# Kernel tuning notes

Measured on AMD Instinct MI355X. Metric: run time of the kernel, lower is better.

## Reference

```python
import jax, jax.numpy as jnp
import numpy as np

B = 2
D_MODEL = 256
D_FFN = 1024
N_LEVELS = 4
N_HEADS = 8
N_POINTS = 4
D_HEAD = D_MODEL // N_HEADS
SHAPES = np.array([[128, 128], [64, 64], [32, 32], [16, 16]], dtype=np.int32)  # (H, W) per level
LEN = int(SHAPES.prod(axis=1).sum())  # 21760
EPS = 1e-5


def _layer_norm(x, g, b):
    m = jnp.mean(x, axis=-1, keepdims=True)
    v = jnp.mean(jnp.square(x - m), axis=-1, keepdims=True)
    return (x - m) * jax.lax.rsqrt(v + EPS) * g + b


def _bilinear_gather(v_l, loc, H, W):
    # v_l: [B, H*W, NH, DH]; loc: [B, L, NH, NP, 2] in normalized [0,1] coords (x, y)
    # grid_sample(align_corners=False, padding_mode=zeros) semantics: pixel = loc * size - 0.5
    x = loc[..., 0] * W - 0.5
    y = loc[..., 1] * H - 0.5
    x0 = jnp.floor(x)
    y0 = jnp.floor(y)
    dx = x - x0
    dy = y - y0
    x0i = x0.astype(jnp.int32)
    y0i = y0.astype(jnp.int32)
    b_ix = jnp.arange(v_l.shape[0])[:, None, None, None]
    h_ix = jnp.arange(v_l.shape[2])[None, None, :, None]

    def corner(xi, yi, w):
        valid = (xi >= 0) & (xi < W) & (yi >= 0) & (yi < H)
        idx = jnp.clip(yi, 0, H - 1) * W + jnp.clip(xi, 0, W - 1)
        v = v_l[b_ix, idx, h_ix]  # [B, L, NH, NP, DH]
        return v * (w * valid.astype(v.dtype))[..., None]

    return (corner(x0i, y0i, (1 - dx) * (1 - dy))
            + corner(x0i + 1, y0i, dx * (1 - dy))
            + corner(x0i, y0i + 1, (1 - dx) * dy)
            + corner(x0i + 1, y0i + 1, dx * dy))


def _forward(src, pos, reference_points,
             w_off, b_off, w_attn, b_attn, w_val, b_val, w_out, b_out,
             ln1_g, ln1_b, w1, b1, w2, b2, ln2_g, ln2_b,
             spatial_shapes, level_start_index, padding_mask):
    shapes = np.asarray(spatial_shapes)        # static per-level (H, W)
    starts = np.asarray(level_start_index)     # static level offsets
    Bsz, L, _ = src.shape

    # ---- MSDeformAttn ----
    q = src + pos                              # with_pos_embed
    value = src @ w_val + b_val
    value = jnp.where(padding_mask[..., None], 0.0, value)
    value = value.reshape(Bsz, L, N_HEADS, D_HEAD)

    off = (q @ w_off + b_off).reshape(Bsz, L, N_HEADS, N_LEVELS, N_POINTS, 2)
    attn = (q @ w_attn + b_attn).reshape(Bsz, L, N_HEADS, N_LEVELS * N_POINTS)
    attn = jax.nn.softmax(attn, axis=-1).reshape(Bsz, L, N_HEADS, N_LEVELS, N_POINTS)

    wh = jnp.asarray(shapes[:, ::-1].copy(), dtype=src.dtype)  # [NL, 2] = (W, H)
    loc = reference_points[:, :, None, :, None, :] + off / wh[None, None, None, :, None, :]

    out = jnp.zeros((Bsz, L, N_HEADS, D_HEAD), src.dtype)
    for l in range(N_LEVELS):
        H, W = int(shapes[l, 0]), int(shapes[l, 1])
        s = int(starts[l])
        v_l = value[:, s:s + H * W]                          # [B, H*W, NH, DH]
        sampled = _bilinear_gather(v_l, loc[:, :, :, l], H, W)  # [B, L, NH, NP, DH]
        out = out + (sampled * attn[:, :, :, l][..., None]).sum(axis=3)
    attn_out = out.reshape(Bsz, L, D_MODEL) @ w_out + b_out

    # ---- residual + LN + FFN + residual + LN (dropout = identity in eval) ----
    x = _layer_norm(src + attn_out, ln1_g, ln1_b)
    ffn = jax.nn.relu(x @ w1 + b1) @ w2 + b2
    return _layer_norm(x + ffn, ln2_g, ln2_b)


def setup_inputs() -> dict:
    key = jax.random.key(0)
    ks = jax.random.split(key, 16)
    s = 0.02
    n_off = N_HEADS * N_LEVELS * N_POINTS
    level_start = np.concatenate([[0], SHAPES.prod(axis=1).cumsum()[:-1]]).astype(np.int32)
    return {
        "src": jax.random.normal(ks[0], (B, LEN, D_MODEL), jnp.float32),
        "pos": jax.random.normal(ks[1], (B, LEN, D_MODEL), jnp.float32),
        "reference_points": jax.random.uniform(ks[2], (B, LEN, N_LEVELS, 2), jnp.float32),
        "spatial_shapes": jnp.asarray(SHAPES),
        "level_start_index": jnp.asarray(level_start),
        "padding_mask": jnp.zeros((B, LEN), jnp.bool_),
        "w_off": jax.random.normal(ks[3], (D_MODEL, n_off * 2), jnp.float32) * s,
        "b_off": jax.random.normal(ks[4], (n_off * 2,), jnp.float32) * 0.5,
        "w_attn": jax.random.normal(ks[5], (D_MODEL, n_off), jnp.float32) * s,
        "b_attn": jnp.zeros((n_off,), jnp.float32),
        "w_val": jax.random.normal(ks[6], (D_MODEL, D_MODEL), jnp.float32) * s,
        "b_val": jnp.zeros((D_MODEL,), jnp.float32),
        "w_out": jax.random.normal(ks[7], (D_MODEL, D_MODEL), jnp.float32) * s,
        "b_out": jnp.zeros((D_MODEL,), jnp.float32),
        "ln1_g": jnp.ones((D_MODEL,), jnp.float32),
        "ln1_b": jnp.zeros((D_MODEL,), jnp.float32),
        "w1": jax.random.normal(ks[8], (D_MODEL, D_FFN), jnp.float32) * s,
        "b1": jnp.zeros((D_FFN,), jnp.float32),
        "w2": jax.random.normal(ks[9], (D_FFN, D_MODEL), jnp.float32) * s,
        "b2": jnp.zeros((D_MODEL,), jnp.float32),
        "ln2_g": jnp.ones((D_MODEL,), jnp.float32),
        "ln2_b": jnp.zeros((D_MODEL,), jnp.float32),
    }


def reference(src, pos, reference_points, spatial_shapes, level_start_index, padding_mask,
              w_off, b_off, w_attn, b_attn, w_val, b_val, w_out, b_out,
              ln1_g, ln1_b, w1, b1, w2, b2, ln2_g, ln2_b):
    return _forward(src, pos, reference_points,
                    w_off, b_off, w_attn, b_attn, w_val, b_val, w_out, b_out,
                    ln1_g, ln1_b, w1, b1, w2, b2, ln2_g, ln2_b,
                    spatial_shapes, level_start_index, padding_mask)
```

## Files before the change

kernel.cpp:

```cpp
#include <hip/hip_runtime.h>
#include <hip/hip_bf16.h>

#define BSZ      2
#define LTOK     21760
#define NTOK     (BSZ * LTOK)
#define DMODEL   256
#define DFFN     1024

typedef __attribute__((ext_vector_type(8))) short short8;
typedef __attribute__((ext_vector_type(4))) float f32x4;

__device__ __forceinline__ unsigned short f2bf(float x) {
    __hip_bfloat16 h = __float2bfloat16(x);
    return *reinterpret_cast<unsigned short*>(&h);
}
__device__ __forceinline__ float bf2f(unsigned short u) {
    union { unsigned int i; float f; } c; c.i = ((unsigned int)u) << 16; return c.f;
}
__device__ __forceinline__ float bflo(unsigned int u) {
    union { unsigned int i; float f; } c; c.i = u << 16; return c.f;
}
__device__ __forceinline__ float bfhi(unsigned int u) {
    union { unsigned int i; float f; } c; c.i = u & 0xffff0000u; return c.f;
}

__device__ __forceinline__ void gload_lds16(const void* g, void* l) {
    __builtin_amdgcn_global_load_lds(
        (const __attribute__((address_space(1))) unsigned int*)g,
        (__attribute__((address_space(3))) unsigned int*)l, 16, 0, 0);
}

#define TM 128
#define TN 256
#define TBK 32
#define EBS 264

__device__ __forceinline__ void gemm_core(
    const unsigned short* __restrict__ A,
    const unsigned short* __restrict__ Bt,
    unsigned short* smem,
    int bm, int bn, int N, int K,
    int tid, int lane, int wm, int wn,
    f32x4 acc[4][4])
{
    const int sr = tid >> 6;
    const int fr = lane & 15;
    const int fk = (lane >> 4) * 8;

    const unsigned short* aR  = A  + (size_t)(bm + sr * 16 + fr) * K + fk;
    const unsigned short* bR0 = Bt + (size_t)min(bn + sr * 16 + fr,       N - 1) * K + fk;
    const unsigned short* bR1 = Bt + (size_t)min(bn + (sr + 8) * 16 + fr, N - 1) * K + fk;

    unsigned short* sA = smem;
    unsigned short* sB = smem + TM * TBK;

    for (int k0 = 0; k0 < K; k0 += TBK) {
        gload_lds16(aR  + k0, &sA[sr * 512]);
        gload_lds16(bR0 + k0, &sB[sr * 512]);
        gload_lds16(bR1 + k0, &sB[(sr + 8) * 512]);
        __syncthreads();

        short8 af[4], bfr[4];
        #pragma unroll
        for (int i = 0; i < 4; ++i)
            af[i] = *(const short8*)&sA[(wm * 4 + i) * 512 + lane * 8];
        #pragma unroll
        for (int j = 0; j < 4; ++j)
            bfr[j] = *(const short8*)&sB[(wn * 4 + j) * 512 + lane * 8];
        #pragma unroll
        for (int i = 0; i < 4; ++i)
            #pragma unroll
            for (int j = 0; j < 4; ++j)
                acc[i][j] = __builtin_amdgcn_mfma_f32_16x16x32_bf16(
                    af[i], bfr[j], acc[i][j], 0, 0, 0);
        __syncthreads();
    }
}

__global__ __launch_bounds__(512, 4) void gemm_mfma(
    const unsigned short* __restrict__ A,
    const unsigned short* __restrict__ Bt, const float* __restrict__ bias,
    unsigned short* __restrict__ Cb,
    int M, int N, int K, int relu)
{
    __shared__ __align__(16) unsigned short smem[TM * TBK + TN * TBK];
    const int tid  = threadIdx.x;
    const int lane = tid & 63;
    const int wave = tid >> 6;
    const int wm = wave >> 2, wn = wave & 3;
    const int bm = blockIdx.y * TM;
    const int bn = blockIdx.x * TN;

    f32x4 acc[4][4];
    #pragma unroll
    for (int i = 0; i < 4; ++i)
        #pragma unroll
        for (int j = 0; j < 4; ++j)
            acc[i][j] = (f32x4){0.f, 0.f, 0.f, 0.f};

    gemm_core(A, Bt, smem, bm, bn, N, K, tid, lane, wm, wn, acc);

    const int r0 = (lane >> 4) * 4;
    const int c0 = lane & 15;
    unsigned short* eb = smem;
    #pragma unroll
    for (int i = 0; i < 4; ++i) {
        if (i) __syncthreads();
        #pragma unroll
        for (int j = 0; j < 4; ++j) {
            const int col = bn + wn * 64 + j * 16 + c0;
            const float bj = (col < N) ? bias[col] : 0.f;
            #pragma unroll
            for (int r = 0; r < 4; ++r) {
                float v = acc[i][j][r] + bj;
                if (relu) v = fmaxf(v, 0.f);
                eb[(wm * 16 + r0 + r) * EBS + wn * 64 + j * 16 + c0] = f2bf(v);
            }
        }
        __syncthreads();
        #pragma unroll
        for (int qq = 0; qq < 2; ++qq) {
            const int q  = tid + qq * 512;
            const int rl = q >> 5;
            const int ch = q & 31;
            const int grow = bm + (rl >> 4) * 64 + i * 16 + (rl & 15);
            const int colb = bn + ch * 8;
            if (colb < N)
                *(uint4*)&Cb[(size_t)grow * N + colb] =
                    *(const uint4*)&eb[rl * EBS + ch * 8];
        }
    }
}

__global__ __launch_bounds__(512, 4) void gemm_proj(
    const unsigned short* __restrict__ A0, const unsigned short* __restrict__ B0,
    const float* __restrict__ bias0, unsigned short* __restrict__ C0,
    const unsigned char* __restrict__ mask,
    const unsigned short* __restrict__ A1, const unsigned short* __restrict__ B1,
    const float* __restrict__ bias1, unsigned short* __restrict__ C1)
{
    __shared__ __align__(16) unsigned short smem[TM * TBK + TN * TBK];
    const int tid  = threadIdx.x;
    const int lane = tid & 63;
    const int wave = tid >> 6;
    const int wm = wave >> 2, wn = wave & 3;
    const int bm = blockIdx.y * TM;
    const int bx = blockIdx.x;

    const int isv = (bx == 0);
    const unsigned short* A    = isv ? A0 : A1;
    const unsigned short* Bt   = isv ? B0 : B1;
    const float*          bias = isv ? bias0 : bias1;
    const int N  = isv ? 256 : 384;
    const int bn = isv ? 0 : (bx - 1) * 256;
    const int K  = 256;

    f32x4 acc[4][4];
    #pragma unroll
    for (int i = 0; i < 4; ++i)
        #pragma unroll
        for (int j = 0; j < 4; ++j)
            acc[i][j] = (f32x4){0.f, 0.f, 0.f, 0.f};

    gemm_core(A, Bt, smem, bm, bn, N, K, tid, lane, wm, wn, acc);

    const int r0 = (lane >> 4) * 4;
    const int c0 = lane & 15;
    unsigned short* eb = smem;
    #pragma unroll
    for (int i = 0; i < 4; ++i) {
        if (i) __syncthreads();
        #pragma unroll
        for (int j = 0; j < 4; ++j) {
            const int col = bn + wn * 64 + j * 16 + c0;
            const float bj = (col < N) ? bias[col] : 0.f;
            #pragma unroll
            for (int r = 0; r < 4; ++r) {
                const int row = bm + wm * 64 + i * 16 + r0 + r;
                float v = acc[i][j][r] + bj;
                if (isv && mask[row]) v = 0.f;
                eb[(wm * 16 + r0 + r) * EBS + wn * 64 + j * 16 + c0] = f2bf(v);
            }
        }
        __syncthreads();
        #pragma unroll
        for (int qq = 0; qq < 2; ++qq) {
            const int q  = tid + qq * 512;
            const int rl = q >> 5;
            const int ch = q & 31;
            const int grow = bm + (rl >> 4) * 64 + i * 16 + (rl & 15);
            const int colb = bn + ch * 8;
            if (colb < N) {
                const uint4 val = *(const uint4*)&eb[rl * EBS + ch * 8];
                if (isv) {
                    const int bb   = grow >= LTOK;
                    const int srow = grow - bb * LTOK;
                    const int hcol = ch >> 2;
                    const int d    = (ch & 3) * 8;
                    *(uint4*)&C0[((size_t)(bb * 8 + hcol) * LTOK + srow) * 32 + d] = val;
                } else {
                    *(uint4*)&C1[(size_t)grow * 384 + colb] = val;
                }
            }
        }
    }
}

__global__ __launch_bounds__(512, 4) void gemm_ln(
    const unsigned short* __restrict__ A,
    const unsigned short* __restrict__ Bt, const float* __restrict__ bias,
    const unsigned short* __restrict__ resid,
    const float* __restrict__ g, const float* __restrict__ be,
    float* __restrict__ outF, unsigned short* __restrict__ outB, int K)
{
    __shared__ __align__(16) unsigned short smem[TM * TBK + TN * TBK];
    const int tid  = threadIdx.x;
    const int lane = tid & 63;
    const int wave = tid >> 6;
    const int wm = wave >> 2, wn = wave & 3;
    const int bm = blockIdx.y * TM;

    f32x4 acc[4][4];
    #pragma unroll
    for (int i = 0; i < 4; ++i)
        #pragma unroll
        for (int j = 0; j < 4; ++j)
            acc[i][j] = (f32x4){0.f, 0.f, 0.f, 0.f};

    gemm_core(A, Bt, smem, bm, 0, 256, K, tid, lane, wm, wn, acc);

    const int r0 = (lane >> 4) * 4;
    const int c0 = lane & 15;
    unsigned short* eb = smem;

    #pragma unroll
    for (int i = 0; i < 4; ++i) {
        if (i) __syncthreads();
        #pragma unroll
        for (int j = 0; j < 4; ++j) {
            const int col = wn * 64 + j * 16 + c0;
            const float bj = bias[col];
            #pragma unroll
            for (int r = 0; r < 4; ++r)
                eb[(wm * 16 + r0 + r) * EBS + col] = f2bf(acc[i][j][r] + bj);
        }
        __syncthreads();

        const int row = tid >> 4;
        const int l   = tid & 15;
        const int grow = bm + (row >> 4) * 64 + i * 16 + (row & 15);
        const unsigned short* rr = resid + (size_t)grow * 256 + l * 16;

        float s = 0.f, sq = 0.f;
        #pragma unroll
        for (int k = 0; k < 2; ++k) {
            const uint4 e = *(const uint4*)&eb[row * EBS + l * 16 + k * 8];
            const uint4 rv = *(const uint4*)(rr + k * 8);
            const unsigned int eu[4] = {e.x, e.y, e.z, e.w};
            const unsigned int ru[4] = {rv.x, rv.y, rv.z, rv.w};
            #pragma unroll
            for (int q = 0; q < 4; ++q) {
                const float v0 = bflo(eu[q]) + bflo(ru[q]);
                const float v1 = bfhi(eu[q]) + bfhi(ru[q]);
                s += v0 + v1;
                sq += v0 * v0 + v1 * v1;
            }
        }
        #pragma unroll
        for (int m = 8; m; m >>= 1) {
            s  += __shfl_xor(s, m, 16);
            sq += __shfl_xor(sq, m, 16);
        }
        const float mean = s * (1.f / 256.f);
        const float var  = sq * (1.f / 256.f) - mean * mean;
        const float rs   = rsqrtf(var + 1e-5f);

        #pragma unroll
        for (int k = 0; k < 2; ++k) {
            const int col = l * 16 + k * 8;
            const uint4 e = *(const uint4*)&eb[row * EBS + col];
            const uint4 rv = *(const uint4*)(rr + k * 8);
            const unsigned int eu[4] = {e.x, e.y, e.z, e.w};
            const unsigned int ru[4] = {rv.x, rv.y, rv.z, rv.w};
            float o[8];
            #pragma unroll
            for (int q = 0; q < 4; ++q) {
                const float g0 = g[col + q * 2],     b0 = be[col + q * 2];
                const float g1 = g[col + q * 2 + 1], b1 = be[col + q * 2 + 1];
                o[q * 2]     = (bflo(eu[q]) + bflo(ru[q]) - mean) * rs * g0 + b0;
                o[q * 2 + 1] = (bfhi(eu[q]) + bfhi(ru[q]) - mean) * rs * g1 + b1;
            }
            if (outB) {
                uint4 pk;
                pk.x = (unsigned)f2bf(o[0]) | ((unsigned)f2bf(o[1]) << 16);
                pk.y = (unsigned)f2bf(o[2]) | ((unsigned)f2bf(o[3]) << 16);
                pk.z = (unsigned)f2bf(o[4]) | ((unsigned)f2bf(o[5]) << 16);
                pk.w = (unsigned)f2bf(o[6]) | ((unsigned)f2bf(o[7]) << 16);
                *(uint4*)(outB + (size_t)grow * 256 + col) = pk;
            } else {
                float4 f0 = make_float4(o[0], o[1], o[2], o[3]);
                float4 f1 = make_float4(o[4], o[5], o[6], o[7]);
                *(float4*)(outF + (size_t)grow * 256 + col) = f0;
                *(float4*)(outF + (size_t)grow * 256 + col + 4) = f1;
            }
        }
        __syncthreads();
    }
}

__global__ __launch_bounds__(256) void prepass(
    const float* __restrict__ src, const float* __restrict__ pos,
    unsigned short* __restrict__ sb, unsigned short* __restrict__ qs)
{
    const size_t i = ((size_t)blockIdx.x * 256 + threadIdx.x) * 4;
    const float4 s = *(const float4*)(src + i);
    const float4 p = *(const float4*)(pos + i);
    ushort4 us, uq;
    us.x = f2bf(s.x); us.y = f2bf(s.y); us.z = f2bf(s.z); us.w = f2bf(s.w);
    uq.x = f2bf(s.x + p.x); uq.y = f2bf(s.y + p.y);
    uq.z = f2bf(s.z + p.z); uq.w = f2bf(s.w + p.w);
    *(ushort4*)(sb + i) = us;
    *(ushort4*)(qs + i) = uq;
}

__global__ void transpose_all(
    const float* __restrict__ w_val, const float* __restrict__ w_off,
    const float* __restrict__ w_att, const float* __restrict__ w_out,
    const float* __restrict__ w1,    const float* __restrict__ w2,
    const float* __restrict__ b_off, const float* __restrict__ b_att,
    unsigned short* __restrict__ wvalT, unsigned short* __restrict__ woaT,
    unsigned short* __restrict__ woutT, unsigned short* __restrict__ w1T,
    unsigned short* __restrict__ w2T,   float* __restrict__ bcat)
{
    const int blk = blockIdx.x;
    const int tx = threadIdx.x, ty = threadIdx.y;
    if (blk == 736) {
        const int t = ty * 32 + tx;
        bcat[t] = (t < 256) ? b_off[t] : b_att[t - 256];
        if (t + 256 < 384) bcat[t + 256] = b_att[t];
        return;
    }
    const float* W; unsigned short* Wt; int K, N, base;
    if      (blk < 64)  { W = w_val; Wt = wvalT;           K = 256;  N = 256;  base = 0;   }
    else if (blk < 128) { W = w_off; Wt = woaT;            K = 256;  N = 256;  base = 64;  }
    else if (blk < 160) { W = w_att; Wt = woaT + 256*256;  K = 256;  N = 128;  base = 128; }
    else if (blk < 224) { W = w_out; Wt = woutT;           K = 256;  N = 256;  base = 160; }
    else if (blk < 480) { W = w1;    Wt = w1T;             K = 256;  N = 1024; base = 224; }
    else                { W = w2;    Wt = w2T;             K = 1024; N = 256;  base = 480; }
    const int local = blk - base;
    const int kb = local % (K / 32);
    const int nb = local / (K / 32);
    const int k0 = kb * 32, n0 = nb * 32;

    __shared__ float t[32][33];
    #pragma unroll
    for (int i = 0; i < 32; i += 8)
        t[ty + i][tx] = W[(size_t)(k0 + ty + i) * N + n0 + tx];
    __syncthreads();
    #pragma unroll
    for (int i = 0; i < 32; i += 8)
        Wt[(size_t)(n0 + ty + i) * K + k0 + tx] = f2bf(t[tx][ty + i]);
}

__global__ __launch_bounds__(256) void sample_kernel(
    const unsigned short* __restrict__ vT, const unsigned short* __restrict__ qp,
    const float* __restrict__ ref,
    const int* __restrict__ sshapes, const int* __restrict__ lstart,
    unsigned short* __restrict__ samp)
{
    __shared__ __align__(16) int   s_o[256][4];
    __shared__ __align__(16) float s_w[256][4];

    const int blk   = blockIdx.x;
    const int plane = blk & 15;
    const int chunk = blk >> 4;
    const int b = plane >> 3;
    const int h = plane & 7;
    const int s0 = chunk * 16;
    const int t = threadIdx.x;

    {
        const int tl = t >> 4;
        const int p  = t & 15;
        const int l  = p >> 2;
        const int pp = p & 3;
        const int H = sshapes[2 * l], W = sshapes[2 * l + 1];
        const float Wf = (float)W, Hf = (float)H;
        const size_t tok = (size_t)(b * LTOK + s0 + tl);

        const float ox = bf2f(qp[tok * 384 + h * 32 + l * 8 + pp * 2 + 0]);
        const float oy = bf2f(qp[tok * 384 + h * 32 + l * 8 + pp * 2 + 1]);
        const float rx = ref[tok * 8 + l * 2 + 0];
        const float ry = ref[tok * 8 + l * 2 + 1];

        const float x = (rx + ox / Wf) * Wf - 0.5f;
        const float y = (ry + oy / Hf) * Hf - 0.5f;
        const float x0 = floorf(x), y0 = floorf(y);
        const float dx = x - x0, dy = y - y0;
        const int x0i = (int)x0, y0i = (int)y0;
        const int s = lstart[l];

        const float a = bf2f(qp[tok * 384 + 256 + h * 16 + p]);
        float mx = a;
        #pragma unroll
        for (int m = 8; m; m >>= 1) mx = fmaxf(mx, __shfl_xor(mx, m, 16));
        const float e = __expf(a - mx);
        float ssum = e;
        #pragma unroll
        for (int m = 8; m; m >>= 1) ssum += __shfl_xor(ssum, m, 16);
        const float prob = e / ssum;

        const float cw[4] = {(1.f - dx) * (1.f - dy), dx * (1.f - dy),
                             (1.f - dx) * dy,         dx * dy};
        const int cx[4] = {x0i, x0i + 1, x0i,     x0i + 1};
        const int cy[4] = {y0i, y0i,     y0i + 1, y0i + 1};
        int4   o4;
        float4 w4;
        #pragma unroll
        for (int c = 0; c < 4; ++c) {
            const bool valid = (cx[c] >= 0) & (cx[c] < W) & (cy[c] >= 0) & (cy[c] < H);
            const int xi = min(max(cx[c], 0), W - 1);
            const int yi = min(max(cy[c], 0), H - 1);
            ((int*)&o4)[c]   = (s + yi * W + xi) * 64;
            ((float*)&w4)[c] = valid ? cw[c] * prob : 0.f;
        }
        const int r = p * 16 + tl;
        *(int4*)&s_o[r][0]   = o4;
        *(float4*)&s_w[r][0] = w4;
    }
    __syncthreads();

    const int tl = t >> 4;
    const int dp = t & 15;
    const char* vp = (const char*)(vT + (size_t)plane * LTOK * 32) + dp * 4;
    float acc0 = 0.f, acc1 = 0.f;
    #pragma unroll
    for (int p = 0; p < 16; ++p) {
        const int r = p * 16 + tl;
        const int4   o4 = *(const int4*)&s_o[r][0];
        const float4 w4 = *(const float4*)&s_w[r][0];
        const unsigned int u0 = *(const unsigned int*)(vp + o4.x);
        const unsigned int u1 = *(const unsigned int*)(vp + o4.y);
        const unsigned int u2 = *(const unsigned int*)(vp + o4.z);
        const unsigned int u3 = *(const unsigned int*)(vp + o4.w);
        acc0 = fmaf(w4.x, bflo(u0), acc0); acc1 = fmaf(w4.x, bfhi(u0), acc1);
        acc0 = fmaf(w4.y, bflo(u1), acc0); acc1 = fmaf(w4.y, bfhi(u1), acc1);
        acc0 = fmaf(w4.z, bflo(u2), acc0); acc1 = fmaf(w4.z, bfhi(u2), acc1);
        acc0 = fmaf(w4.w, bflo(u3), acc0); acc1 = fmaf(w4.w, bfhi(u3), acc1);
    }
    const unsigned int o = (unsigned)f2bf(acc0) | ((unsigned)f2bf(acc1) << 16);
    *(unsigned int*)(samp + (size_t)(b * LTOK + s0 + tl) * 256 + h * 32 + dp * 2) = o;
}

extern "C" void kernel_launch(void* const* d_in, const int* in_sizes, int n_in,
                              void* d_out, int out_size, void* d_ws, size_t ws_size,
                              hipStream_t stream)
{
    const float* src   = (const float*)d_in[0];
    const float* pos   = (const float*)d_in[1];
    const float* ref   = (const float*)d_in[2];
    const int*   sshap = (const int*)d_in[3];
    const int*   lstrt = (const int*)d_in[4];
    const unsigned char* mask = (const unsigned char*)d_in[5];
    const float* w_off = (const float*)d_in[6];
    const float* b_off = (const float*)d_in[7];
    const float* w_att = (const float*)d_in[8];
    const float* b_att = (const float*)d_in[9];
    const float* w_val = (const float*)d_in[10];
    const float* b_val = (const float*)d_in[11];
    const float* w_out = (const float*)d_in[12];
    const float* b_out = (const float*)d_in[13];
    const float* ln1g  = (const float*)d_in[14];
    const float* ln1b  = (const float*)d_in[15];
    const float* w1    = (const float*)d_in[16];
    const float* b1    = (const float*)d_in[17];
    const float* w2    = (const float*)d_in[18];
    const float* b2    = (const float*)d_in[19];
    const float* ln2g  = (const float*)d_in[20];
    const float* ln2b  = (const float*)d_in[21];
    float* out = (float*)d_out;

    const size_t HSZ = (size_t)NTOK * 256 * 2;
    char* w = (char*)d_ws;
    unsigned short* qs     = (unsigned short*)w;
    unsigned short* samp16 = (unsigned short*)w;
    unsigned short* qpb    = (unsigned short*)(w + HSZ);
    unsigned short* vT     = (unsigned short*)(w + HSZ * 5 / 2);
    unsigned short* hidb   = (unsigned short*)w;
    unsigned short* sb     = (unsigned short*)(w + HSZ * 9 / 2);
    unsigned short* xb     = (unsigned short*)(w + HSZ * 11 / 2);
    char* wreg = w + HSZ * 13 / 2;
    unsigned short* wvalT  = (unsigned short*)wreg;
    unsigned short* woaT   = wvalT + 256 * 256;
    unsigned short* woutT  = woaT + 384 * 256;
    unsigned short* w1T    = woutT + 256 * 256;
    unsigned short* w2T    = w1T + 1024 * 256;
    float*          bcat   = (float*)(w2T + 256 * 1024);

    const dim3 blk(256);
    const dim3 blk512(512);

    prepass<<<dim3(NTOK / 4), blk, 0, stream>>>(src, pos, sb, qs);

    transpose_all<<<dim3(737), dim3(32, 8), 0, stream>>>(
        w_val, w_off, w_att, w_out, w1, w2, b_off, b_att,
        wvalT, woaT, woutT, w1T, w2T, bcat);

    gemm_proj<<<dim3(3, NTOK / TM), blk512, 0, stream>>>(
        sb, wvalT, b_val, vT, mask, qs, woaT, bcat, qpb);

    sample_kernel<<<dim3(16 * (LTOK / 16)), blk, 0, stream>>>(
        vT, qpb, ref, sshap, lstrt, samp16);

    gemm_ln<<<dim3(1, NTOK / TM), blk512, 0, stream>>>(
        samp16, woutT, b_out, sb, ln1g, ln1b, nullptr, xb, 256);

    gemm_mfma<<<dim3(4, NTOK / TM), blk512, 0, stream>>>(
        xb, w1T, b1, hidb, NTOK, DFFN, 256, 1);

    gemm_ln<<<dim3(1, NTOK / TM), blk512, 0, stream>>>(
        hidb, w2T, b2, xb, ln2g, ln2b, out, nullptr, DFFN);
}
```

Baseline: 463.5 us.

## Rewrite GEMM+LayerNorm kernels to keep full weight tile in LDS and stream A

Replaces the tiled gemm_ln with a templated kernel that stages a 256-column by 256-K chunk of the weight matrix in a 128KB shared buffer. Each wave reads its own 16-row A fragment straight from global memory into MFMA operands, with no A staging through LDS. The LayerNorm epilogue becomes per-wave, four lanes per row, with no block-wide syncs. This aims to cut A-tile LDS traffic and epilogue synchronisation. In exchange occupancy drops to one block per CU, and global A loads go without LDS buffering or prefetch.

```diff
diff --git a/kernel.cpp b/kernel.cpp
--- a/kernel.cpp
+++ b/kernel.cpp
@@ -206,105 +206,121 @@
     }
 }
 
-__global__ __launch_bounds__(512, 4) void gemm_ln(
+template<int KFULL, int KCHUNKS>
+__global__ __launch_bounds__(512, 1) void gemm_ln_bres(
     const unsigned short* __restrict__ A,
     const unsigned short* __restrict__ Bt, const float* __restrict__ bias,
     const unsigned short* __restrict__ resid,
     const float* __restrict__ g, const float* __restrict__ be,
-    float* __restrict__ outF, unsigned short* __restrict__ outB, int K)
-{
-    __shared__ __align__(16) unsigned short smem[TM * TBK + TN * TBK];
+    float* __restrict__ outF, unsigned short* __restrict__ outB)
+{
+    __shared__ __align__(16) unsigned short smem[65536];
     const int tid  = threadIdx.x;
     const int lane = tid & 63;
     const int wave = tid >> 6;
-    const int wm = wave >> 2, wn = wave & 3;
-    const int bm = blockIdx.y * TM;
-
-    f32x4 acc[4][4];
-    #pragma unroll
-    for (int i = 0; i < 4; ++i)
-        #pragma unroll
-        for (int j = 0; j < 4; ++j)
-            acc[i][j] = (f32x4){0.f, 0.f, 0.f, 0.f};
-
-    gemm_core(A, Bt, smem, bm, 0, 256, K, tid, lane, wm, wn, acc);
-
+    const int fr = lane & 15;
+    const int fk = (lane >> 4) * 8;
+    const int arow = blockIdx.x * 128 + wave * 16;
+
+    const unsigned short* aP = A + (size_t)(arow + fr) * KFULL + fk;
+
+    f32x4 acc[16];
+    #pragma unroll
+    for (int j = 0; j < 16; ++j) acc[j] = (f32x4){0.f, 0.f, 0.f, 0.f};
+
+    for (int kc = 0; kc < KCHUNKS; ++kc) {
+        if (kc) __syncthreads();
+        #pragma unroll
+        for (int idx = 0; idx < 16; ++idx) {
+            const int f  = wave * 16 + idx;
+            const int ks = f >> 4;
+            const int j  = f & 15;
+            const uint4 v = *(const uint4*)(Bt + (size_t)(j * 16 + fr) * KFULL
+                                            + kc * 256 + ks * 32 + fk);
+            *(uint4*)&smem[f * 512 + lane * 8] = v;
+        }
+        __syncthreads();
+
+        #pragma unroll
+        for (int ks = 0; ks < 8; ++ks) {
+            const short8 a = *(const short8*)(aP + kc * 256 + ks * 32);
+            #pragma unroll
+            for (int j = 0; j < 16; ++j) {
+                const short8 b = *(const short8*)&smem[(ks * 16 + j) * 512 + lane * 8];
+                acc[j] = __builtin_amdgcn_mfma_f32_16x16x32_bf16(a, b, acc[j], 0, 0, 0);
+            }
+        }
+    }
+    __syncthreads();
+
+    unsigned short* ew = &smem[wave * 4224];
     const int r0 = (lane >> 4) * 4;
-    const int c0 = lane & 15;
-    unsigned short* eb = smem;
-
-    #pragma unroll
-    for (int i = 0; i < 4; ++i) {
-        if (i) __syncthreads();
-        #pragma unroll
-        for (int j = 0; j < 4; ++j) {
-            const int col = wn * 64 + j * 16 + c0;
-            const float bj = bias[col];
-            #pragma unroll
-            for (int r = 0; r < 4; ++r)
-                eb[(wm * 16 + r0 + r) * EBS + col] = f2bf(acc[i][j][r] + bj);
-        }
-        __syncthreads();
-
-        const int row = tid >> 4;
-        const int l   = tid & 15;
-        const int grow = bm + (row >> 4) * 64 + i * 16 + (row & 15);
-        const unsigned short* rr = resid + (size_t)grow * 256 + l * 16;
-
-        float s = 0.f, sq = 0.f;
-        #pragma unroll
-        for (int k = 0; k < 2; ++k) {
-            const uint4 e = *(const uint4*)&eb[row * EBS + l * 16 + k * 8];
-            const uint4 rv = *(const uint4*)(rr + k * 8);
-            const unsigned int eu[4] = {e.x, e.y, e.z, e.w};
-            const unsigned int ru[4] = {rv.x, rv.y, rv.z, rv.w};
-            #pragma unroll
-            for (int q = 0; q < 4; ++q) {
-                const float v0 = bflo(eu[q]) + bflo(ru[q]);
-                const float v1 = bfhi(eu[q]) + bfhi(ru[q]);
-                s += v0 + v1;
-                sq += v0 * v0 + v1 * v1;
-            }
-        }
-        #pragma unroll
-        for (int m = 8; m; m >>= 1) {
-            s  += __shfl_xor(s, m, 16);
-            sq += __shfl_xor(sq, m, 16);
-        }
-        const float mean = s * (1.f / 256.f);
-        const float var  = sq * (1.f / 256.f) - mean * mean;
-        const float rs   = rsqrtf(var + 1e-5f);
-
-        #pragma unroll
-        for (int k = 0; k < 2; ++k) {
-            const int col = l * 16 + k * 8;
-            const uint4 e = *(const uint4*)&eb[row * EBS + col];
-            const uint4 rv = *(const uint4*)(rr + k * 8);
-            const unsigned int eu[4] = {e.x, e.y, e.z, e.w};
-            const unsigned int ru[4] = {rv.x, rv.y, rv.z, rv.w};
-            float o[8];
-            #pragma unroll
-            for (int q = 0; q < 4; ++q) {
-                const float g0 = g[col + q * 2],     b0 = be[col + q * 2];
-                const float g1 = g[col + q * 2 + 1], b1 = be[col + q * 2 + 1];
-                o[q * 2]     = (bflo(eu[q]) + bflo(ru[q]) - mean) * rs * g0 + b0;
-                o[q * 2 + 1] = (bfhi(eu[q]) + bfhi(ru[q]) - mean) * rs * g1 + b1;
-            }
-            if (outB) {
-                uint4 pk;
-                pk.x = (unsigned)f2bf(o[0]) | ((unsigned)f2bf(o[1]) << 16);
-                pk.y = (unsigned)f2bf(o[2]) | ((unsigned)f2bf(o[3]) << 16);
-                pk.z = (unsigned)f2bf(o[4]) | ((unsigned)f2bf(o[5]) << 16);
-                pk.w = (unsigned)f2bf(o[6]) | ((unsigned)f2bf(o[7]) << 16);
-                *(uint4*)(outB + (size_t)grow * 256 + col) = pk;
-            } else {
-                float4 f0 = make_float4(o[0], o[1], o[2], o[3]);
-                float4 f1 = make_float4(o[4], o[5], o[6], o[7]);
-                *(float4*)(outF + (size_t)grow * 256 + col) = f0;
-                *(float4*)(outF + (size_t)grow * 256 + col + 4) = f1;
-            }
-        }
-        __syncthreads();
+    const int c0 = fr;
+    #pragma unroll
+    for (int j = 0; j < 16; ++j) {
+        const float bj = bias[j * 16 + c0];
+        #pragma unroll
+        for (int r = 0; r < 4; ++r)
+            ew[(r0 + r) * 264 + j * 16 + c0] = f2bf(acc[j][r] + bj);
+    }
+
+    const int row = lane >> 2;
+    const int l   = lane & 3;
+    const int grow = arow + row;
+    const unsigned short* rr = resid + (size_t)grow * 256 + l * 64;
+
+    float s = 0.f, sq = 0.f;
+    #pragma unroll
+    for (int k = 0; k < 8; ++k) {
+        const uint4 e  = *(const uint4*)&ew[row * 264 + l * 64 + k * 8];
+        const uint4 rv = *(const uint4*)(rr + k * 8);
+        const unsigned int eu[4] = {e.x, e.y, e.z, e.w};
+        const unsigned int ru[4] = {rv.x, rv.y, rv.z, rv.w};
+        #pragma unroll
+        for (int q = 0; q < 4; ++q) {
+            const float v0 = bflo(eu[q]) + bflo(ru[q]);
+            const float v1 = bfhi(eu[q]) + bfhi(ru[q]);
+            s += v0 + v1;
+            sq += v0 * v0 + v1 * v1;
+        }
+    }
+    #pragma unroll
+    for (int m = 2; m; m >>= 1) {
+        s  += __shfl_xor(s, m, 4);
+        sq += __shfl_xor(sq, m, 4);
+    }
+    const float mean = s * (1.f / 256.f);
+    const float var  = sq * (1.f / 256.f) - mean * mean;
+    const float rs   = rsqrtf(var + 1e-5f);
+
+    #pragma unroll
+    for (int k = 0; k < 8; ++k) {
+        const int col = l * 64 + k * 8;
+        const uint4 e  = *(const uint4*)&ew[row * 264 + col];
+        const uint4 rv = *(const uint4*)(rr + k * 8);
+        const unsigned int eu[4] = {e.x, e.y, e.z, e.w};
+        const unsigned int ru[4] = {rv.x, rv.y, rv.z, rv.w};
+        float o[8];
+        #pragma unroll
+        for (int q = 0; q < 4; ++q) {
+            const float g0 = g[col + q * 2],     b0 = be[col + q * 2];
+            const float g1 = g[col + q * 2 + 1], b1 = be[col + q * 2 + 1];
+            o[q * 2]     = (bflo(eu[q]) + bflo(ru[q]) - mean) * rs * g0 + b0;
+            o[q * 2 + 1] = (bfhi(eu[q]) + bfhi(ru[q]) - mean) * rs * g1 + b1;
+        }
+        if (outB) {
+            uint4 pk;
+            pk.x = (unsigned)f2bf(o[0]) | ((unsigned)f2bf(o[1]) << 16);
+            pk.y = (unsigned)f2bf(o[2]) | ((unsigned)f2bf(o[3]) << 16);
+            pk.z = (unsigned)f2bf(o[4]) | ((unsigned)f2bf(o[5]) << 16);
+            pk.w = (unsigned)f2bf(o[6]) | ((unsigned)f2bf(o[7]) << 16);
+            *(uint4*)(outB + (size_t)grow * 256 + col) = pk;
+        } else {
+            float4 f0 = make_float4(o[0], o[1], o[2], o[3]);
+            float4 f1 = make_float4(o[4], o[5], o[6], o[7]);
+            *(float4*)(outF + (size_t)grow * 256 + col) = f0;
+            *(float4*)(outF + (size_t)grow * 256 + col + 4) = f1;
+        }
     }
 }
 
@@ -512,12 +528,12 @@
     sample_kernel<<<dim3(16 * (LTOK / 16)), blk, 0, stream>>>(
         vT, qpb, ref, sshap, lstrt, samp16);
 
-    gemm_ln<<<dim3(1, NTOK / TM), blk512, 0, stream>>>(
-        samp16, woutT, b_out, sb, ln1g, ln1b, nullptr, xb, 256);
+    gemm_ln_bres<256, 1><<<dim3(NTOK / 128), blk512, 0, stream>>>(
+        samp16, woutT, b_out, sb, ln1g, ln1b, nullptr, xb);
 
     gemm_mfma<<<dim3(4, NTOK / TM), blk512, 0, stream>>>(
         xb, w1T, b1, hidb, NTOK, DFFN, 256, 1);
 
-    gemm_ln<<<dim3(1, NTOK / TM), blk512, 0, stream>>>(
-        hidb, w2T, b2, xb, ln2g, ln2b, out, nullptr, DFFN);
-}
+    gemm_ln_bres<1024, 4><<<dim3(NTOK / 128), blk512, 0, stream>>>(
+        hidb, w2T, b2, xb, ln2g, ln2b, out, nullptr);
+}
```

Measured after the change: 510.7 us. +10.2%, slower.
